# Kernel optimization log

Hardware: AMD Instinct MI355X
Metric: run time of the kernel (lower is better)

## Reference

```python
import jax, jax.numpy as jnp
import numpy as np

B, S, DIM, SDIM = 4, 4096, 1024, 256


def setup_inputs() -> dict:
    key = jax.random.key(0)
    ks = jax.random.split(key, 10)
    def lin(k, din, dout):
        return jax.random.normal(k, (din, dout), jnp.float32) / np.float32(np.sqrt(din))
    return {
        "x": jax.random.normal(ks[0], (B, S, DIM), jnp.float32),
        "ln_g": jnp.ones((DIM,), jnp.float32),
        "ln_b": jnp.zeros((DIM,), jnp.float32),
        "mix_w": jax.random.normal(ks[1], (DIM, 1, 3), jnp.float32) * 0.3,  # depthwise conv kernel
        "mix_b": jnp.zeros((DIM,), jnp.float32),
        "Wi": lin(ks[2], DIM, DIM), "bi": jnp.zeros((DIM,), jnp.float32),
        "Wsin": lin(ks[3], DIM, SDIM), "bsin": jnp.zeros((SDIM,), jnp.float32),
        "Wd": lin(ks[4], DIM, SDIM), "bd": jnp.zeros((SDIM,), jnp.float32),
        "Wsel": lin(ks[5], DIM, SDIM), "bsel": jnp.zeros((SDIM,), jnp.float32),
        "Wso": lin(ks[6], SDIM, DIM), "bso": jnp.zeros((DIM,), jnp.float32),
        "Wg": lin(ks[7], DIM, DIM), "bg": jnp.zeros((DIM,), jnp.float32),
        "Wout": lin(ks[8], DIM, DIM), "bout": jnp.zeros((DIM,), jnp.float32),
    }


def reference(x, ln_g, ln_b, mix_w, mix_b, Wi, bi, Wsin, bsin, Wd, bd,
              Wsel, bsel, Wso, bso, Wg, bg, Wout, bout):
    eps = 1e-5
    # LayerNorm over last dim
    mu = jnp.mean(x, axis=-1, keepdims=True)
    var = jnp.mean(jnp.square(x - mu), axis=-1, keepdims=True)
    h = (x - mu) * jax.lax.rsqrt(var + eps) * ln_g + ln_b
    # depthwise Conv1d, kernel=3, padding=1, groups=dim
    hc = jnp.transpose(h, (0, 2, 1))  # [B, C, L]
    mixed = jax.lax.conv_general_dilated(
        hc, mix_w, window_strides=(1,), padding=[(1, 1)],
        dimension_numbers=("NCH", "OIH", "NCH"), feature_group_count=hc.shape[1])
    mixed = jnp.transpose(mixed + mix_b[None, :, None], (0, 2, 1))  # [B, S, D]
    u = jnp.tanh(mixed @ Wi + bi)                 # [B, S, D]
    x_state = jnp.tanh(mixed @ Wsin + bsin)       # [B, S, N]
    decay = jax.nn.sigmoid(mixed @ Wd + bd)       # [B, S, N]
    select = jax.nn.sigmoid(mixed @ Wsel + bsel)  # [B, S, N]
    # sequential linear recurrence: state = d*state + (1-d)*x_state
    def step(state, inp):
        dt, xt = inp
        state = dt * state + (1.0 - dt) * xt
        return state, state
    init = jnp.zeros((x.shape[0], x_state.shape[-1]), x.dtype)
    _, states = jax.lax.scan(step, init,
                             (jnp.swapaxes(decay, 0, 1), jnp.swapaxes(x_state, 0, 1)))
    states = jnp.swapaxes(states, 0, 1)           # [B, S, N]
    y = (select * states) @ Wso + bso             # [B, S, D]
    g = jax.nn.sigmoid(mixed @ Wg + bg)
    out = (g * y + (1.0 - g) * u) @ Wout + bout
    return x + out
```

## Files before the change

kernel.cpp:

```cpp
#include <hip/hip_runtime.h>
#include <hip/hip_bf16.h>
#include <math.h>

typedef __bf16 bf16_t;
typedef __bf16 bf16x8 __attribute__((ext_vector_type(8)));
typedef __bf16 bf16x4 __attribute__((ext_vector_type(4)));
typedef float  f32x4  __attribute__((ext_vector_type(4)));

#define B_ 4
#define S_ 4096
#define D_ 1024
#define N_ 256
#define M_ (B_*S_)

__device__ __forceinline__ float fsig(float x){
    return __builtin_amdgcn_rcpf(1.0f + __expf(-x));
}
__device__ __forceinline__ float ftanh(float x){
    return 1.0f - 2.0f*__builtin_amdgcn_rcpf(1.0f + __expf(2.0f*x));
}

__device__ __forceinline__ void gload_lds16(const void* g, void* l){
    __builtin_amdgcn_global_load_lds(
        (const __attribute__((address_space(1))) unsigned int*)g,
        (__attribute__((address_space(3))) unsigned int*)l, 16, 0, 0);
}

struct TJobs {
    const float* in[7];
    bf16_t*      out[7];
    int R[7];
    int C[7];
};

__global__ void transpose_all(TJobs j){
    int z = blockIdx.z;
    int R = j.R[z], C = j.C[z];
    int c0 = blockIdx.x*32, r0 = blockIdx.y*32;
    if (c0 >= C || r0 >= R) return;
    __shared__ float tile[32][33];
    int tx = threadIdx.x, ty = threadIdx.y;
    const float* in = j.in[z];
    bf16_t* out = j.out[z];
    #pragma unroll
    for (int i=0;i<32;i+=8)
        tile[ty+i][tx] = in[(size_t)(r0+ty+i)*C + (c0+tx)];
    __syncthreads();
    #pragma unroll
    for (int i=0;i<32;i+=8)
        out[(size_t)(c0+ty+i)*R + (r0+tx)] = (bf16_t)tile[tx][ty+i];
}

__global__ void ln_kernel(const float* __restrict__ x, const float* __restrict__ gw,
                          const float* __restrict__ bw, bf16_t* __restrict__ h){
    int row = blockIdx.x;
    int t = threadIdx.x;
    float4 v = ((const float4*)(x + (size_t)row*D_))[t];
    float s = v.x+v.y+v.z+v.w;
    float q = v.x*v.x+v.y*v.y+v.z*v.z+v.w*v.w;
    #pragma unroll
    for (int o=1;o<64;o<<=1){ s += __shfl_xor(s,o,64); q += __shfl_xor(q,o,64); }
    __shared__ float sw[4], sq[4];
    int wid = t>>6;
    if ((t&63)==0){ sw[wid]=s; sq[wid]=q; }
    __syncthreads();
    s = sw[0]+sw[1]+sw[2]+sw[3];
    q = sq[0]+sq[1]+sq[2]+sq[3];
    float mu = s*(1.0f/D_);
    float rs = rsqrtf(q*(1.0f/D_) - mu*mu + 1e-5f);
    float4 gv = ((const float4*)gw)[t];
    float4 bv = ((const float4*)bw)[t];
    bf16x4 o4;
    o4[0] = (bf16_t)((v.x-mu)*rs*gv.x + bv.x);
    o4[1] = (bf16_t)((v.y-mu)*rs*gv.y + bv.y);
    o4[2] = (bf16_t)((v.z-mu)*rs*gv.z + bv.z);
    o4[3] = (bf16_t)((v.w-mu)*rs*gv.w + bv.w);
    *(bf16x4*)(h + (size_t)row*D_ + t*4) = o4;
}

__global__ void conv_kernel(const bf16_t* __restrict__ h, const float* __restrict__ w,
                            const float* __restrict__ mb, bf16_t* __restrict__ mix){
    int idx = blockIdx.x*256 + threadIdx.x;
    int g8  = idx & 127;
    int row = idx >> 7;
    int s   = row & (S_-1);
    int d0  = g8*8;
    const bf16_t* hr = h + (size_t)row*D_ + d0;
    bf16x8 cur = *(const bf16x8*)hr;
    bf16x8 prv, nxt;
    #pragma unroll
    for (int i=0;i<8;i++){ prv[i]=(bf16_t)0.0f; nxt[i]=(bf16_t)0.0f; }
    if (s > 0)      prv = *(const bf16x8*)(hr - D_);
    if (s < S_-1)   nxt = *(const bf16x8*)(hr + D_);
    bf16x8 ov;
    #pragma unroll
    for (int i=0;i<8;i++){
        int d = d0+i;
        float o = (float)prv[i]*w[d*3] + (float)cur[i]*w[d*3+1] + (float)nxt[i]*w[d*3+2] + mb[d];
        ov[i] = (bf16_t)o;
    }
    *(bf16x8*)(mix + (size_t)row*D_ + d0) = ov;
}

struct Epi {
    const float *b0,*b1,*b2,*b3,*b4;
    bf16_t *u, *g, *z;
    bf16_t *xs, *dc, *sel;
    const bf16_t *gbuf, *ubuf;
    const float *resid;
    float *outp;
};

#define WAITV3()  asm volatile("s_waitcnt vmcnt(3)" ::: "memory")
#define WAITV0()  asm volatile("s_waitcnt vmcnt(0)" ::: "memory")
#define WAITLGK0() asm volatile("s_waitcnt lgkmcnt(0)" ::: "memory")
#define CFENCE()  asm volatile("" ::: "memory")
#define BARR()    __builtin_amdgcn_s_barrier()

template<int MODE>
__global__ __launch_bounds__(512,4)
void gemm128(const bf16_t* __restrict__ A, const bf16_t* __restrict__ Bt,
             int K, Epi e){
    extern __shared__ __align__(16) char lds[];
    const int ATILE = 8192;
    const int BTILE = 16384;
    int t = threadIdx.x;
    int wave = t>>6, lane = t&63;
    int wm = (wave>>2)*64;
    int wn = (wave&3)*64;
    int lm = lane&15, quad = lane>>4;

    int m0 = blockIdx.x*128;
    int n0 = blockIdx.y*256;
    int NT = K>>5;

    const bf16_t* gA = A  + (size_t)(m0 + (t>>2))*K + (t&3)*8;
    const bf16_t* gB = Bt + (size_t)(n0 + (t>>2))*K + (t&3)*8;

    auto stage = [&](int kt, int buf){
        const bf16_t* a = gA + kt*32;
        const bf16_t* b = gB + kt*32;
        char* da = lds + buf*ATILE + t*16;
        char* db = lds + 16384 + buf*BTILE + t*16;
        gload_lds16(a, da);
        gload_lds16(b, db);
        gload_lds16(b + (size_t)128*K, db + 8192);
    };

    int raBase = (wm+lm)*64 + quad*16;
    int rbBase = (wn+lm)*64 + quad*16;

    f32x4 acc[4][4];
    #pragma unroll
    for (int i=0;i<4;i++)
        #pragma unroll
        for (int j=0;j<4;j++)
            #pragma unroll
            for (int r=0;r<4;r++) acc[i][j][r]=0.0f;

    bf16x8 aF[4], bF[4];

    stage(0,0);
    stage(1,1);
    WAITV3();
    BARR();
    CFENCE();

    for (int kt=0; kt<NT; ++kt){
        int buf = kt&1;
        const char* pa = lds + buf*ATILE + raBase;
        const char* pb = lds + 16384 + buf*BTILE + rbBase;

        #pragma unroll
        for (int j=0;j<4;j++) bF[j] = *(const bf16x8*)(pb + j*1024);
        #pragma unroll
        for (int i=0;i<4;i++) aF[i] = *(const bf16x8*)(pa + i*1024);

        #pragma unroll
        for (int i=0;i<4;i++)
            #pragma unroll
            for (int j=0;j<4;j++)
                acc[i][j] = __builtin_amdgcn_mfma_f32_16x16x32_bf16(aF[i], bF[j], acc[i][j], 0,0,0);

        WAITLGK0();
        BARR();
        CFENCE();
        if (kt+2 < NT){
            stage(kt+2, buf);
            WAITV3();
            BARR();
            CFENCE();
        } else if (kt+1 < NT){
            WAITV0();
            BARR();
            CFENCE();
        }
    }
    __syncthreads();

    if (MODE==0 || MODE==1){
        const float* bp = e.b0; int cbase = 0; bf16_t* dst = 0; int width = D_;
        bool ut = true;
        if (MODE==0){
            ut = (n0 < 1280);
            if (n0 < 1024){ bp=e.b0; cbase=n0; dst=e.u; width=D_; }
            else if (n0 < 1792){
                int sub=(n0-1024)>>8;
                bp  = sub==0? e.b1 : sub==1? e.b2 : e.b3;
                dst = sub==0? e.xs : sub==1? e.dc : e.sel;
                cbase = 0; width = N_;
            } else { bp=e.b4; cbase=n0-1792; dst=e.g; width=D_; }
        } else {
            bp = e.b0; cbase = n0; width = D_;
        }
        bf16_t* Tb = (bf16_t*)lds;
        #pragma unroll
        for (int h=0; h<2; h++){
            if (h) __syncthreads();
            if (wm == h*64){
                #pragma unroll
                for (int ii=0;ii<4;ii++){
                    #pragma unroll
                    for (int j=0;j<4;j++){
                        float bv = bp[(MODE==0?cbase:n0) + wn + j*16 + lm];
                        #pragma unroll
                        for (int r=0;r<4;r++){
                            float v = acc[ii][j][r] + bv;
                            if (MODE==0) v = ut ? ftanh(v) : fsig(v);
                            Tb[(ii*16+quad*4+r)*260 + wn + j*16 + lm] = (bf16_t)v;
                        }
                    }
                }
            }
            __syncthreads();
            if (MODE==0){
                #pragma unroll
                for (int it=0; it<4; it++){
                    int idx = it*512 + t;
                    int row = idx>>5, c8 = idx&31;
                    bf16x8 v = *(const bf16x8*)&Tb[row*260 + c8*8];
                    *(bf16x8*)&dst[(size_t)(m0 + h*64 + row)*width + cbase + c8*8] = v;
                }
            } else {
                #pragma unroll
                for (int it=0; it<4; it++){
                    int idx = it*512 + t;
                    int row = idx>>5, c8 = idx&31;
                    bf16x8 y = *(const bf16x8*)&Tb[row*260 + c8*8];
                    size_t gi = (size_t)(m0 + h*64 + row)*D_ + n0 + c8*8;
                    bf16x8 gv = *(const bf16x8*)&e.gbuf[gi];
                    bf16x8 uv = *(const bf16x8*)&e.ubuf[gi];
                    bf16x8 o;
                    #pragma unroll
                    for (int q=0;q<8;q++){
                        float gf = (float)gv[q];
                        o[q] = (bf16_t)(gf*(float)y[q] + (1.0f-gf)*(float)uv[q]);
                    }
                    *(bf16x8*)&e.z[gi] = o;
                }
            }
        }
    } else {
        float* T = (float*)lds;
        #pragma unroll
        for (int pZ=0; pZ<4; pZ++){
            if (pZ) __syncthreads();
            if (wm == (pZ>>1)*64){
                int ib = (pZ&1)*2;
                #pragma unroll
                for (int ii=0;ii<2;ii++){
                    #pragma unroll
                    for (int j=0;j<4;j++)
                        #pragma unroll
                        for (int r=0;r<4;r++)
                            T[(ii*16+quad*4+r)*260 + wn + j*16 + lm] = acc[ib+ii][j][r];
                }
            }
            __syncthreads();
            #pragma unroll
            for (int it=0; it<4; it++){
                int idx = it*512 + t;
                int row = idx>>6, c4 = idx&63;
                f32x4 v = *(const f32x4*)&T[row*260 + c4*4];
                size_t gi = (size_t)(m0 + pZ*32 + row)*D_ + n0 + c4*4;
                float4 res = *(const float4*)&e.resid[gi];
                float4 bb  = *(const float4*)&e.b0[n0 + c4*4];
                float4 o;
                o.x = v[0]+res.x+bb.x; o.y = v[1]+res.y+bb.y;
                o.z = v[2]+res.z+bb.z; o.w = v[3]+res.w+bb.w;
                *(float4*)&e.outp[gi] = o;
            }
        }
    }
}

__global__ void scan_p1(const bf16_t* __restrict__ dc, const bf16_t* __restrict__ xs,
                        float* __restrict__ aggA, float* __restrict__ aggB){
    int wg4 = blockIdx.x*4 + (threadIdx.x>>6);
    int b = wg4>>6, ch = wg4&63;
    int l4 = (threadIdx.x&63)*4;
    size_t base = ((size_t)b*S_ + ch*64)*N_ + l4;
    float A0=1.f,A1=1.f,A2=1.f,A3=1.f, B0=0.f,B1=0.f,B2=0.f,B3=0.f;
    for (int t=0;t<64;t++){
        bf16x4 d4 = *(const bf16x4*)(dc + base + (size_t)t*N_);
        bf16x4 x4 = *(const bf16x4*)(xs + base + (size_t)t*N_);
        float d;
        d=(float)d4[0]; A0*=d; B0=d*B0+(1.f-d)*(float)x4[0];
        d=(float)d4[1]; A1*=d; B1=d*B1+(1.f-d)*(float)x4[1];
        d=(float)d4[2]; A2*=d; B2=d*B2+(1.f-d)*(float)x4[2];
        d=(float)d4[3]; A3*=d; B3=d*B3+(1.f-d)*(float)x4[3];
    }
    size_t o = (size_t)wg4*N_ + l4;
    float4 av; av.x=A0; av.y=A1; av.z=A2; av.w=A3;
    float4 bv; bv.x=B0; bv.y=B1; bv.z=B2; bv.w=B3;
    *(float4*)(aggA+o) = av;
    *(float4*)(aggB+o) = bv;
}

__global__ void scan_p2(const float* __restrict__ aggA, const float* __restrict__ aggB,
                        float* __restrict__ pre){
    int b = blockIdx.x, n = threadIdx.x;
    float s = 0.0f;
    for (int ch=0; ch<64; ch++){
        size_t i = ((size_t)b*64+ch)*N_+n;
        pre[i] = s;
        s = aggA[i]*s + aggB[i];
    }
}

__global__ void scan_p3(const bf16_t* __restrict__ dc, const bf16_t* __restrict__ xs,
                        const bf16_t* __restrict__ sel, const float* __restrict__ pre,
                        bf16_t* __restrict__ ss){
    int wg4 = blockIdx.x*4 + (threadIdx.x>>6);
    int b = wg4>>6, ch = wg4&63;
    int l4 = (threadIdx.x&63)*4;
    size_t base = ((size_t)b*S_ + ch*64)*N_ + l4;
    size_t o = (size_t)wg4*N_ + l4;
    float4 pv = *(const float4*)(pre+o);
    float s0=pv.x, s1=pv.y, s2=pv.z, s3=pv.w;
    for (int t=0;t<64;t++){
        size_t i = base + (size_t)t*N_;
        bf16x4 d4 = *(const bf16x4*)(dc+i);
        bf16x4 x4 = *(const bf16x4*)(xs+i);
        bf16x4 e4 = *(const bf16x4*)(sel+i);
        float d;
        d=(float)d4[0]; s0=d*s0+(1.f-d)*(float)x4[0];
        d=(float)d4[1]; s1=d*s1+(1.f-d)*(float)x4[1];
        d=(float)d4[2]; s2=d*s2+(1.f-d)*(float)x4[2];
        d=(float)d4[3]; s3=d*s3+(1.f-d)*(float)x4[3];
        bf16x4 o4;
        o4[0]=(bf16_t)((float)e4[0]*s0);
        o4[1]=(bf16_t)((float)e4[1]*s1);
        o4[2]=(bf16_t)((float)e4[2]*s2);
        o4[3]=(bf16_t)((float)e4[3]*s3);
        *(bf16x4*)(ss+i) = o4;
    }
}

extern "C" void kernel_launch(void* const* d_in, const int* in_sizes, int n_in,
                              void* d_out, int out_size, void* d_ws, size_t ws_size,
                              hipStream_t stream){
    const float* x    = (const float*)d_in[0];
    const float* ln_g = (const float*)d_in[1];
    const float* ln_b = (const float*)d_in[2];
    const float* mixw = (const float*)d_in[3];
    const float* mixb = (const float*)d_in[4];
    const float* Wi   = (const float*)d_in[5];
    const float* bi   = (const float*)d_in[6];
    const float* Wsin = (const float*)d_in[7];
    const float* bsin = (const float*)d_in[8];
    const float* Wd   = (const float*)d_in[9];
    const float* bd   = (const float*)d_in[10];
    const float* Wsel = (const float*)d_in[11];
    const float* bsel = (const float*)d_in[12];
    const float* Wso  = (const float*)d_in[13];
    const float* bso  = (const float*)d_in[14];
    const float* Wg   = (const float*)d_in[15];
    const float* bg   = (const float*)d_in[16];
    const float* Wout = (const float*)d_in[17];
    const float* bout = (const float*)d_in[18];
    float* out = (float*)d_out;

    char* p = (char*)d_ws;
    auto alloc = [&](size_t bytes)->char*{ char* r=p; p += (bytes+255)&~(size_t)255; return r; };
    bf16_t* hB    = (bf16_t*)alloc((size_t)M_*D_*2);
    bf16_t* mixB  = (bf16_t*)alloc((size_t)M_*D_*2);
    bf16_t* uB    = (bf16_t*)alloc((size_t)M_*D_*2);
    bf16_t* gB    = (bf16_t*)alloc((size_t)M_*D_*2);
    bf16_t* ssB   = (bf16_t*)alloc((size_t)M_*N_*2);
    bf16_t* xs    = (bf16_t*)alloc((size_t)M_*N_*2);
    bf16_t* dc    = (bf16_t*)alloc((size_t)M_*N_*2);
    bf16_t* sel   = (bf16_t*)alloc((size_t)M_*N_*2);
    bf16_t* WbigT = (bf16_t*)alloc((size_t)2816*1024*2);
    bf16_t* WsoT  = (bf16_t*)alloc(1024*256*2);
    bf16_t* WoutT = (bf16_t*)alloc(1024*1024*2);
    float*  aggA  = (float*)alloc((size_t)4*64*256*4);
    float*  aggB  = (float*)alloc((size_t)4*64*256*4);
    float*  pre   = (float*)alloc((size_t)4*64*256*4);
    bf16_t* zB = mixB;

    TJobs tj;
    tj.in[0]=Wi;   tj.out[0]=WbigT;            tj.R[0]=1024; tj.C[0]=1024;
    tj.in[1]=Wsin; tj.out[1]=WbigT+1024*1024;  tj.R[1]=1024; tj.C[1]=256;
    tj.in[2]=Wd;   tj.out[2]=WbigT+1280*1024;  tj.R[2]=1024; tj.C[2]=256;
    tj.in[3]=Wsel; tj.out[3]=WbigT+1536*1024;  tj.R[3]=1024; tj.C[3]=256;
    tj.in[4]=Wg;   tj.out[4]=WbigT+(size_t)1792*1024; tj.R[4]=1024; tj.C[4]=1024;
    tj.in[5]=Wso;  tj.out[5]=WsoT;             tj.R[5]=256;  tj.C[5]=1024;
    tj.in[6]=Wout; tj.out[6]=WoutT;            tj.R[6]=1024; tj.C[6]=1024;
    transpose_all<<<dim3(32,32,7), dim3(32,8), 0, stream>>>(tj);

    ln_kernel  <<<M_, 256, 0, stream>>>(x, ln_g, ln_b, hB);
    conv_kernel<<<M_*128/256, 256, 0, stream>>>(hB, mixw, mixb, mixB);

    Epi e0 = {};
    e0.b0=bi; e0.b1=bsin; e0.b2=bd; e0.b3=bsel; e0.b4=bg;
    e0.u=uB; e0.g=gB; e0.xs=xs; e0.dc=dc; e0.sel=sel;
    gemm128<0><<<dim3(M_/128, 11), 512, 49152, stream>>>(mixB, WbigT, 1024, e0);

    scan_p1<<<64, 256, 0, stream>>>(dc, xs, aggA, aggB);
    scan_p2<<<4,  256, 0, stream>>>(aggA, aggB, pre);
    scan_p3<<<64, 256, 0, stream>>>(dc, xs, sel, pre, ssB);

    Epi e1 = {};
    e1.b0=bso; e1.gbuf=gB; e1.ubuf=uB; e1.z=zB;
    gemm128<1><<<dim3(M_/128, 4), 512, 49152, stream>>>(ssB, WsoT, 256, e1);

    Epi e2 = {};
    e2.b0=bout; e2.resid=x; e2.outp=out;
    gemm128<2><<<dim3(M_/128, 4), 512, 49152, stream>>>(zB, WoutT, 1024, e2);
}
```

Before: 407.6 us.

## Triple-buffer GEMM LDS tiles and prefetch next fragments during MFMAs

Moves the GEMM main loop from a double-buffered to a triple-buffered LDS pipeline with a static 72KB shared array. It also software-pipelines the fragment reads, loading the next k-tile's A/B fragments from LDS while the current MFMAs run, and drops one barrier per iteration. The goal is to hide global-to-LDS and LDS-to-register latency behind matrix math. The cost is more LDS per block, which may limit how many 512-thread blocks fit per CU, plus more register pressure.

```diff
diff --git a/kernel.cpp b/kernel.cpp
--- a/kernel.cpp
+++ b/kernel.cpp
@@ -121,9 +121,7 @@
 __global__ __launch_bounds__(512,4)
 void gemm128(const bf16_t* __restrict__ A, const bf16_t* __restrict__ Bt,
              int K, Epi e){
-    extern __shared__ __align__(16) char lds[];
-    const int ATILE = 8192;
-    const int BTILE = 16384;
+    __shared__ __align__(16) char lds[73728];
     int t = threadIdx.x;
     int wave = t>>6, lane = t&63;
     int wm = (wave>>2)*64;
@@ -137,11 +135,12 @@
     const bf16_t* gA = A  + (size_t)(m0 + (t>>2))*K + (t&3)*8;
     const bf16_t* gB = Bt + (size_t)(n0 + (t>>2))*K + (t&3)*8;
 
-    auto stage = [&](int kt, int buf){
+    auto stage = [&](int kt){
+        int x = kt % 3;
         const bf16_t* a = gA + kt*32;
         const bf16_t* b = gB + kt*32;
-        char* da = lds + buf*ATILE + t*16;
-        char* db = lds + 16384 + buf*BTILE + t*16;
+        char* da = lds + x*8192  + t*16;
+        char* db = lds + 24576 + x*16384 + t*16;
         gload_lds16(a, da);
         gload_lds16(b, db);
         gload_lds16(b + (size_t)128*K, db + 8192);
@@ -160,40 +159,48 @@
 
     bf16x8 aF[4], bF[4];
 
-    stage(0,0);
-    stage(1,1);
+    stage(0);
+    stage(1);
+    stage(2);
     WAITV3();
     BARR();
     CFENCE();
+    {
+        const char* pa = lds + raBase;
+        const char* pb = lds + 24576 + rbBase;
+        #pragma unroll
+        for (int j=0;j<4;j++) bF[j] = *(const bf16x8*)(pb + j*1024);
+        #pragma unroll
+        for (int i=0;i<4;i++) aF[i] = *(const bf16x8*)(pa + i*1024);
+    }
 
     for (int kt=0; kt<NT; ++kt){
-        int buf = kt&1;
-        const char* pa = lds + buf*ATILE + raBase;
-        const char* pb = lds + 16384 + buf*BTILE + rbBase;
-
-        #pragma unroll
-        for (int j=0;j<4;j++) bF[j] = *(const bf16x8*)(pb + j*1024);
-        #pragma unroll
-        for (int i=0;i<4;i++) aF[i] = *(const bf16x8*)(pa + i*1024);
-
-        #pragma unroll
-        for (int i=0;i<4;i++)
-            #pragma unroll
-            for (int j=0;j<4;j++)
-                acc[i][j] = __builtin_amdgcn_mfma_f32_16x16x32_bf16(aF[i], bF[j], acc[i][j], 0,0,0);
-
         WAITLGK0();
         BARR();
         CFENCE();
-        if (kt+2 < NT){
-            stage(kt+2, buf);
+        if (kt+3 < NT){
+            stage(kt+3);
             WAITV3();
-            BARR();
-            CFENCE();
-        } else if (kt+1 < NT){
+        } else {
             WAITV0();
-            BARR();
-            CFENCE();
+        }
+        CFENCE();
+
+        bool more = (kt+1 < NT);
+        int xn = (kt+1) % 3;
+        const char* pan = lds + xn*8192  + raBase;
+        const char* pbn = lds + 24576 + xn*16384 + rbBase;
+
+        #pragma unroll
+        for (int j=0;j<4;j++){
+            #pragma unroll
+            for (int i=0;i<4;i++)
+                acc[i][j] = __builtin_amdgcn_mfma_f32_16x16x32_bf16(aF[i], bF[j], acc[i][j], 0,0,0);
+            if (more) bF[j] = *(const bf16x8*)(pbn + j*1024);
+        }
+        if (more){
+            #pragma unroll
+            for (int i=0;i<4;i++) aF[i] = *(const bf16x8*)(pan + i*1024);
         }
     }
     __syncthreads();
@@ -415,7 +422,7 @@
     Epi e0 = {};
     e0.b0=bi; e0.b1=bsin; e0.b2=bd; e0.b3=bsel; e0.b4=bg;
     e0.u=uB; e0.g=gB; e0.xs=xs; e0.dc=dc; e0.sel=sel;
-    gemm128<0><<<dim3(M_/128, 11), 512, 49152, stream>>>(mixB, WbigT, 1024, e0);
+    gemm128<0><<<dim3(M_/128, 11), 512, 0, stream>>>(mixB, WbigT, 1024, e0);
 
     scan_p1<<<64, 256, 0, stream>>>(dc, xs, aggA, aggB);
     scan_p2<<<4,  256, 0, stream>>>(aggA, aggB, pre);
@@ -423,9 +430,9 @@
 
     Epi e1 = {};
     e1.b0=bso; e1.gbuf=gB; e1.ubuf=uB; e1.z=zB;
-    gemm128<1><<<dim3(M_/128, 4), 512, 49152, stream>>>(ssB, WsoT, 256, e1);
+    gemm128<1><<<dim3(M_/128, 4), 512, 0, stream>>>(ssB, WsoT, 256, e1);
 
     Epi e2 = {};
     e2.b0=bout; e2.resid=x; e2.outp=out;
-    gemm128<2><<<dim3(M_/128, 4), 512, 49152, stream>>>(zB, WoutT, 1024, e2);
-}
+    gemm128<2><<<dim3(M_/128, 4), 512, 0, stream>>>(zB, WoutT, 1024, e2);
+}
```

Result: no change. 402.3 us (-1.3%).
